# Performance work log

Hardware: AMD Instinct MI355X
Metric: run time of the kernel (lower is better)

The kernel has to match this reference:

```python
import jax, jax.numpy as jnp
import numpy as np

BOS = 1          # BOS_TOK_IDX
PAD = 0          # PAD_TOK_IDX (embedding padding row zeroed)
NL = 2           # n_layers (both decoder and encoder)
H_DEC = 1024     # decoder hidden = enc.emb_size
H_ENC = 512      # encoder hidden per direction (out_size = 1024)


def lstm_cell(x, h, c, Wih, Whh, bih, bhh):
    # PyTorch gate order: i, f, g, o
    gates = x @ Wih.T + h @ Whh.T + bih + bhh
    i, f, g, o = jnp.split(gates, 4, axis=-1)
    c = jax.nn.sigmoid(f) * c + jax.nn.sigmoid(i) * jnp.tanh(g)
    h = jax.nn.sigmoid(o) * jnp.tanh(c)
    return h, c


def setup_inputs() -> dict:
    key = jax.random.key(0)
    ks = jax.random.split(key, 20)
    B, T_ENC, V, E = 32, 128, 32000, 512
    sd = 1.0 / np.sqrt(H_DEC)
    se = 1.0 / np.sqrt(H_ENC)
    u = lambda k, shape, s: jax.random.uniform(k, shape, jnp.float32, -s, s)
    emb_W = jax.random.normal(ks[0], (V, E), jnp.float32)
    emb_W = emb_W.at[PAD].set(0.0)  # padding_idx
    return {
        "enc_outs": jax.random.normal(ks[1], (B, T_ENC, 2 * H_ENC), jnp.float32),
        "enc_h": 0.1 * jax.random.normal(ks[2], (NL, B, H_DEC), jnp.float32),
        "enc_c": 0.1 * jax.random.normal(ks[3], (NL, B, H_DEC), jnp.float32),
        "max_len": 256,
        "emb_W": emb_W,
        # decoder LSTM (unidirectional, 2 layers; layer0 in=E, layer1 in=H_DEC)
        "dec_Wih0": u(ks[4], (4 * H_DEC, E), sd),
        "dec_Whh0": u(ks[5], (4 * H_DEC, H_DEC), sd),
        "dec_bih0": u(ks[6], (4 * H_DEC,), sd),
        "dec_bhh0": u(ks[7], (4 * H_DEC,), sd),
        "dec_Wih1": u(ks[8], (4 * H_DEC, H_DEC), sd),
        "dec_Whh1": u(ks[9], (4 * H_DEC, H_DEC), sd),
        "dec_bih1": u(ks[10], (4 * H_DEC,), sd),
        "dec_bhh1": u(ks[11], (4 * H_DEC,), sd),
        # encoder biLSTM, stacked [layer, dir]; input dim 1024 for both layers
        "enc_Wih": u(ks[12], (NL, 2, 4 * H_ENC, 2 * H_ENC), se),
        "enc_Whh": u(ks[13], (NL, 2, 4 * H_ENC, H_ENC), se),
        "enc_bih": u(ks[14], (NL, 2, 4 * H_ENC), se),
        "enc_bhh": u(ks[15], (NL, 2, 4 * H_ENC), se),
    }


def _run_dir(x, Wih, Whh, bih, bhh, reverse):
    # x: [B, T, D] -> ys: [B, T, H], final (h, c)
    B = x.shape[0]
    H = Whh.shape[-1]
    z = jnp.zeros((B, H), dtype=x.dtype)

    def step(carry, xt):
        h, c = lstm_cell(xt, carry[0], carry[1], Wih, Whh, bih, bhh)
        return (h, c), h

    (hT, cT), ys = jax.lax.scan(step, (z, z), jnp.swapaxes(x, 0, 1), reverse=reverse)
    return jnp.swapaxes(ys, 0, 1), hT, cT


def reference(enc_outs, enc_h, enc_c, max_len, emb_W,
              dec_Wih0, dec_Whh0, dec_bih0, dec_bhh0,
              dec_Wih1, dec_Whh1, dec_bih1, dec_bhh1,
              enc_Wih, enc_Whh, enc_bih, enc_bhh):
    B = enc_outs.shape[0]
    # dec_inps is never updated in the loop: always the BOS embedding (eval dropout = id)
    x0 = jnp.broadcast_to(emb_W[BOS], (B, emb_W.shape[1]))

    def dec_step(carry, _):
        h0, c0, h1, c1 = carry
        h0, c0 = lstm_cell(x0, h0, c0, dec_Wih0, dec_Whh0, dec_bih0, dec_bhh0)
        h1, c1 = lstm_cell(h0, h1, c1, dec_Wih1, dec_Whh1, dec_bih1, dec_bhh1)
        return (h0, c0, h1, c1), h1

    init = (enc_h[0], enc_c[0], enc_h[1], enc_c[1])
    _, result = jax.lax.scan(dec_step, init, None, length=max_len)  # [T, B, H_DEC]
    out = jnp.swapaxes(result, 0, 1)  # [B, T, H_DEC]

    # bidirectional encoder over the decoded sequence (pre_embedded, full lengths)
    for l in range(NL):
        yf, hf, cf = _run_dir(out, enc_Wih[l, 0], enc_Whh[l, 0], enc_bih[l, 0], enc_bhh[l, 0], False)
        yb, hb, cb = _run_dir(out, enc_Wih[l, 1], enc_Whh[l, 1], enc_bih[l, 1], enc_bhh[l, 1], True)
        out = jnp.concatenate([yf, yb], axis=-1)

    # to_dec_state: concat last-layer fwd/bwd states, expand over n_layers
    lnhn = jnp.concatenate([hf, hb], axis=1)  # [B, out_size]
    lncn = jnp.concatenate([cf, cb], axis=1)
    dec_h = jnp.broadcast_to(lnhn, (NL,) + lnhn.shape)
    dec_c = jnp.broadcast_to(lncn, (NL,) + lncn.shape)
    return out, dec_h, dec_c
```

## Files before the change

### kernel.cpp

```cpp
#include <hip/hip_runtime.h>


typedef _Float16 f16;
typedef _Float16 hvec8 __attribute__((ext_vector_type(8)));
typedef float fvec4 __attribute__((ext_vector_type(4)));

#define WS_H0   4096
#define WS_H1   135168
#define WS_HE   266240
#define WS_DEC  397312
#define WS_Y0   17174528

__device__ __forceinline__ fvec4 mf(hvec8 a, hvec8 b, fvec4 c) {
    return __builtin_amdgcn_mfma_f32_16x16x32_f16(a, b, c, 0, 0, 0);
}

__device__ __forceinline__ hvec8 ldb8(const float* p) {
    hvec8 h;
#pragma unroll
    for (int j = 0; j < 8; ++j) h[j] = (f16)p[j];
    return h;
}

__device__ __forceinline__ hvec8 lda8(const f16* p) {
    hvec8 v;
    asm volatile("global_load_dwordx4 %0, %1, off sc1" : "=v"(v) : "v"(p));
    return v;
}
__device__ __forceinline__ void vm_wait() {
    asm volatile("s_waitcnt vmcnt(0)" ::: "memory");
    __builtin_amdgcn_sched_barrier(0);
}

__device__ __forceinline__ void st2(f16* p, float a, float b) {
    union { f16 h[2]; unsigned u; } x;
    x.h[0] = (f16)a; x.h[1] = (f16)b;
    __hip_atomic_store((unsigned*)p, x.u, __ATOMIC_RELAXED, __HIP_MEMORY_SCOPE_AGENT);
}

__device__ __forceinline__ float sigf(float x) { return 1.f / (1.f + __expf(-x)); }
__device__ __forceinline__ float thf(float x) {
    x = fminf(15.f, fmaxf(-15.f, x));
    float e = __expf(2.f * x);
    return (e - 1.f) / (e + 1.f);
}

#define RED(t, m, w, n)  red[(((t)*16 + (m))*132) + ((w)*16) + (n)]

__device__ __forceinline__ float sum8(const float* p) {
    return ((p[0] + p[16]) + (p[32] + p[48])) + ((p[64] + p[80]) + (p[96] + p[112]));
}

__global__ void __launch_bounds__(512, 1)
seq2seq_kernel(const float* __restrict__ enc_h, const float* __restrict__ enc_c,
               const float* __restrict__ emb_W,
               const float* __restrict__ dWih0, const float* __restrict__ dWhh0,
               const float* __restrict__ dbih0, const float* __restrict__ dbhh0,
               const float* __restrict__ dWih1, const float* __restrict__ dWhh1,
               const float* __restrict__ dbih1, const float* __restrict__ dbhh1,
               const float* __restrict__ eWih, const float* __restrict__ eWhh,
               const float* __restrict__ ebih, const float* __restrict__ ebhh,
               float* __restrict__ out, char* __restrict__ ws)
{
    const int tid  = threadIdx.x;
    const int wave = tid >> 6, lane = tid & 63;
    const int wg   = blockIdx.x;
    const int bg   = wg >> 7;
    const int g    = wg & 127;
    const int n16  = lane & 15;
    const int kq   = (lane >> 4) * 8;

    unsigned* flags  = (unsigned*)ws;
    unsigned* myflag = flags + (size_t)wg * 4;

    f16* H0  = (f16*)(ws + WS_H0);
    f16* H1  = (f16*)(ws + WS_H1);
    f16* HE  = (f16*)(ws + WS_HE);
    f16* DEC = (f16*)(ws + WS_DEC);
    f16* Y0  = (f16*)(ws + WS_Y0);

    __shared__ float red[64 * 132];
    __shared__ float cdec[2][8][16];
    __shared__ float cenc[16][16];
    __shared__ float pre0_l[32];
    __shared__ float bias1_l[32];
    __shared__ float biasE_l[64];

    unsigned cnt = 0;
    auto bar = [&](int base, int width) {
        const unsigned tgt = ++cnt;
        __syncthreads();
        if (wave == 0) {
            if (lane == 0)
                __hip_atomic_store(myflag, tgt, __ATOMIC_RELAXED, __HIP_MEMORY_SCOPE_AGENT);
            const unsigned* p0 = flags + (size_t)(base + (lane & (width - 1))) * 4;
            for (;;) {
                unsigned a = __hip_atomic_load(p0, __ATOMIC_RELAXED, __HIP_MEMORY_SCOPE_AGENT);
                if (width > 64) {
                    unsigned b = __hip_atomic_load(p0 + 64 * 4, __ATOMIC_RELAXED, __HIP_MEMORY_SCOPE_AGENT);
                    a = a < b ? a : b;
                    if (width > 128) {
                        unsigned c2 = __hip_atomic_load(p0 + 128 * 4, __ATOMIC_RELAXED, __HIP_MEMORY_SCOPE_AGENT);
                        unsigned d2 = __hip_atomic_load(p0 + 192 * 4, __ATOMIC_RELAXED, __HIP_MEMORY_SCOPE_AGENT);
                        a = a < c2 ? a : c2;
                        a = a < d2 ? a : d2;
                    }
                }
                if (__all((int)(a >= tgt))) break;
            }
        }
        __syncthreads();
    };

    const int u0 = g * 8;
    hvec8 bL0[2][4], bL1[2][8];
    {
        const int gate = n16 >> 2, uu = n16 & 3;
#pragma unroll
        for (int t = 0; t < 2; ++t) {
            const int r = gate * 1024 + u0 + t * 4 + uu;
#pragma unroll
            for (int s = 0; s < 4; ++s)
                bL0[t][s] = ldb8(dWhh0 + (size_t)r * 1024 + wave * 128 + s * 32 + kq);
#pragma unroll
            for (int s = 0; s < 8; ++s) {
                const int k1 = wave * 256 + s * 32;
                bL1[t][s] = (k1 < 1024)
                    ? ldb8(dWih1 + (size_t)r * 1024 + k1 + kq)
                    : ldb8(dWhh1 + (size_t)r * 1024 + (k1 - 1024) + kq);
            }
        }
    }
    if (tid < 128) {
        const int which = tid >> 6, q = tid & 63, j = q >> 4, m = q & 15;
        const int b = bg * 16 + m, u = u0 + 2 * j;
        const float* src_c = enc_c + (size_t)(which * 32 + b) * 1024 + u;
        const float* src_h = enc_h + (size_t)(which * 32 + b) * 1024 + u;
        cdec[which][2 * j][m]     = src_c[0];
        cdec[which][2 * j + 1][m] = src_c[1];
        f16* dst = which ? H1 : H0;
        st2(dst + (size_t)(32 + b) * 1024 + u, src_h[0], src_h[1]);
    }
    if (tid < 32) {
        const int t = tid >> 4, nn = tid & 15;
        const int r = (nn >> 2) * 1024 + u0 + t * 4 + (nn & 3);
        const float* x0 = emb_W + 512;
        float s = dbih0[r] + dbhh0[r];
        const float* wr = dWih0 + (size_t)r * 512;
        for (int k = 0; k < 512; ++k) s += wr[k] * x0[k];
        pre0_l[tid]  = s;
        bias1_l[tid] = dbih1[r] + dbhh1[r];
    }
    bar(bg * 128, 128);

    for (int tau = 0; tau <= 256; ++tau) {
        const int prd = (tau + 1) & 1;
        const int pwr = tau & 1;
        fvec4 acc[4];
#pragma unroll
        for (int i = 0; i < 4; ++i) acc[i] = 0;
        const int m = n16;
        hvec8 a0f[4], a1f[8];
        if (tau < 256) {
            const f16* a0 = H0 + (size_t)(prd * 32 + bg * 16 + m) * 1024 + wave * 128 + kq;
#pragma unroll
            for (int s = 0; s < 4; ++s) a0f[s] = lda8(a0 + s * 32);
        }
        if (tau >= 1) {
            const f16* a1 = (wave < 4)
                ? H0 + (size_t)(prd * 32 + bg * 16 + m) * 1024 + wave * 256 + kq
                : H1 + (size_t)(pwr * 32 + bg * 16 + m) * 1024 + (wave - 4) * 256 + kq;
#pragma unroll
            for (int s = 0; s < 8; ++s) a1f[s] = lda8(a1 + s * 32);
        }
        vm_wait();
        if (tau < 256) {
#pragma unroll
            for (int s = 0; s < 4; ++s) {
                acc[0] = mf(a0f[s], bL0[0][s], acc[0]);
                acc[1] = mf(a0f[s], bL0[1][s], acc[1]);
            }
        }
        if (tau >= 1) {
#pragma unroll
            for (int s = 0; s < 8; ++s) {
                acc[2] = mf(a1f[s], bL1[0][s], acc[2]);
                acc[3] = mf(a1f[s], bL1[1][s], acc[3]);
            }
        }
        {
            const int mg = lane >> 4;
#pragma unroll
            for (int t = 0; t < 4; ++t)
#pragma unroll
                for (int r = 0; r < 4; ++r)
                    RED(t, mg * 4 + r, wave, n16) = acc[t][r];
        }
        __syncthreads();
        if (tid < 64 && tau < 256) {
            const int j = tid >> 4, m2 = tid & 15, t = j >> 1;
            float hh[2];
#pragma unroll
            for (int e = 0; e < 2; ++e) {
                const int uu = 2 * j + e, ul = uu & 3;
                const float* p = &RED(t, m2, 0, ul);
                const float gi = sum8(p)      + pre0_l[t * 16 + ul];
                const float gf = sum8(p + 4)  + pre0_l[t * 16 + 4 + ul];
                const float gg = sum8(p + 8)  + pre0_l[t * 16 + 8 + ul];
                const float go = sum8(p + 12) + pre0_l[t * 16 + 12 + ul];
                float c = cdec[0][uu][m2];
                c = sigf(gf) * c + sigf(gi) * thf(gg);
                hh[e] = sigf(go) * thf(c);
                cdec[0][uu][m2] = c;
            }
            st2(H0 + (size_t)(pwr * 32 + bg * 16 + m2) * 1024 + u0 + 2 * j, hh[0], hh[1]);
        }
        if (tid >= 64 && tid < 128 && tau >= 1) {
            const int q = tid - 64;
            const int j = q >> 4, m2 = q & 15, t = j >> 1;
            float hh[2];
#pragma unroll
            for (int e = 0; e < 2; ++e) {
                const int uu = 2 * j + e, ul = uu & 3;
                const float* p = &RED(2 + t, m2, 0, ul);
                const float gi = sum8(p)      + bias1_l[t * 16 + ul];
                const float gf = sum8(p + 4)  + bias1_l[t * 16 + 4 + ul];
                const float gg = sum8(p + 8)  + bias1_l[t * 16 + 8 + ul];
                const float go = sum8(p + 12) + bias1_l[t * 16 + 12 + ul];
                float c = cdec[1][uu][m2];
                c = sigf(gf) * c + sigf(gi) * thf(gg);
                hh[e] = sigf(go) * thf(c);
                cdec[1][uu][m2] = c;
            }
            const int b = bg * 16 + m2, u = u0 + 2 * j;
            st2(H1 + (size_t)(prd * 32 + b) * 1024 + u, hh[0], hh[1]);
            st2(DEC + ((size_t)(tau - 1) * 32 + b) * 1024 + u, hh[0], hh[1]);
        }
        bar(bg * 128, 128);
    }

    bar(0, 256);
    if (wg >= 128) return;

    const int bg2 = wg >> 6;
    const int dir = (wg >> 5) & 1;
    const int ge  = wg & 31;
    const int ue0 = ge * 16;
    const int dbase = bg2 * 64 + dir * 32;
    for (int l = 0; l < 2; ++l) {
        hvec8 bE[4][6];
        {
            const int gate = n16 >> 2, uu = n16 & 3;
            const float* Wih = eWih + (size_t)(l * 2 + dir) * 2048 * 1024;
            const float* Whh = eWhh + (size_t)(l * 2 + dir) * 2048 * 512;
#pragma unroll
            for (int t = 0; t < 4; ++t) {
                const int r = gate * 512 + ue0 + t * 4 + uu;
#pragma unroll
                for (int s = 0; s < 6; ++s) {
                    const int kb = wave * 192 + s * 32;
                    bE[t][s] = (kb < 1024)
                        ? ldb8(Wih + (size_t)r * 1024 + kb + kq)
                        : ldb8(Whh + (size_t)r * 512 + (kb - 1024) + kq);
                }
            }
        }
        if (tid < 64) {
            const int t = tid >> 4, nn = tid & 15;
            const int r = (nn >> 2) * 512 + ue0 + t * 4 + (nn & 3);
            biasE_l[tid] = ebih[(size_t)(l * 2 + dir) * 2048 + r]
                         + ebhh[(size_t)(l * 2 + dir) * 2048 + r];
        }
        if (tid < 128) {
            const int j = tid >> 4, m = tid & 15;
            cenc[2 * j][m] = 0.f;
            cenc[2 * j + 1][m] = 0.f;
            st2(HE + (size_t)((dir * 2 + 1) * 32 + bg2 * 16 + m) * 512 + ue0 + 2 * j, 0.f, 0.f);
        }
        bar(dbase, 32);
        const f16* yprev = (l == 0) ? DEC : Y0;
        hvec8 ypf[6];
        {
            const int t0 = dir ? 255 : 0;
            const int b = bg2 * 16 + n16;
#pragma unroll
            for (int s = 0; s < 6; ++s) {
                const int kb = wave * 192 + s * 32;
                if (kb < 1024)
                    ypf[s] = lda8(yprev + ((size_t)t0 * 32 + b) * 1024 + kb + kq);
            }
        }
        for (int tau = 0; tau < 256; ++tau) {
            const int t = dir ? (255 - tau) : tau;
            const int prd = (tau + 1) & 1, pwr = tau & 1;
            const int b = bg2 * 16 + n16;
            hvec8 hef[6];
#pragma unroll
            for (int s = 0; s < 6; ++s) {
                const int kb = wave * 192 + s * 32;
                if (kb >= 1024)
                    hef[s] = lda8(HE + (size_t)((dir * 2 + prd) * 32 + b) * 512 + (kb - 1024) + kq);
            }
            vm_wait();
            fvec4 acc2[4];
#pragma unroll
            for (int i = 0; i < 4; ++i) acc2[i] = 0;
#pragma unroll
            for (int s = 0; s < 6; ++s) {
                const int kb = wave * 192 + s * 32;
                const hvec8 a = (kb < 1024) ? ypf[s] : hef[s];
                acc2[0] = mf(a, bE[0][s], acc2[0]);
                acc2[1] = mf(a, bE[1][s], acc2[1]);
                acc2[2] = mf(a, bE[2][s], acc2[2]);
                acc2[3] = mf(a, bE[3][s], acc2[3]);
            }
            if (tau < 255) {
                const int tn = dir ? (t - 1) : (t + 1);
#pragma unroll
                for (int s = 0; s < 6; ++s) {
                    const int kb = wave * 192 + s * 32;
                    if (kb < 1024)
                        ypf[s] = lda8(yprev + ((size_t)tn * 32 + b) * 1024 + kb + kq);
                }
            }
            const int mg = lane >> 4;
#pragma unroll
            for (int tt = 0; tt < 4; ++tt)
#pragma unroll
                for (int r = 0; r < 4; ++r)
                    RED(tt, mg * 4 + r, wave, n16) = acc2[tt][r];
            __syncthreads();
            if (tid < 128) {
                const int j = tid >> 4, m2 = tid & 15;
                float hh[2], cc[2];
#pragma unroll
                for (int e = 0; e < 2; ++e) {
                    const int uu = 2 * j + e, tt = uu >> 2, ul = uu & 3;
                    const float* p = &RED(tt, m2, 0, ul);
                    const float gi = sum8(p)      + biasE_l[tt * 16 + ul];
                    const float gf = sum8(p + 4)  + biasE_l[tt * 16 + 4 + ul];
                    const float gg = sum8(p + 8)  + biasE_l[tt * 16 + 8 + ul];
                    const float go = sum8(p + 12) + biasE_l[tt * 16 + 12 + ul];
                    float c = cenc[uu][m2];
                    c = sigf(gf) * c + sigf(gi) * thf(gg);
                    hh[e] = sigf(go) * thf(c);
                    cc[e] = c;
                    cenc[uu][m2] = c;
                }
                const int b2 = bg2 * 16 + m2, u = ue0 + 2 * j;
                st2(HE + (size_t)((dir * 2 + pwr) * 32 + b2) * 512 + u, hh[0], hh[1]);
                if (l == 0) {
                    st2(Y0 + ((size_t)t * 32 + b2) * 1024 + dir * 512 + u, hh[0], hh[1]);
                } else {
                    float* o = out + ((size_t)b2 * 256 + t) * 1024 + dir * 512 + u;
                    o[0] = hh[0]; o[1] = hh[1];
                    if (tau == 255) {
                        const int col = dir * 512 + u;
                        float* oh = out + 8388608 + (size_t)b2 * 1024 + col;
                        float* oc = out + 8454144 + (size_t)b2 * 1024 + col;
                        oh[0] = hh[0]; oh[1] = hh[1];
                        oh[32768] = hh[0]; oh[32769] = hh[1];
                        oc[0] = cc[0]; oc[1] = cc[1];
                        oc[32768] = cc[0]; oc[32769] = cc[1];
                    }
                }
            }
            bar(dbase, 32);
        }
        if (l == 0) bar(bg2 * 64, 64);
    }
}

extern "C" void kernel_launch(void* const* d_in, const int* in_sizes, int n_in,
                              void* d_out, int out_size, void* d_ws, size_t ws_size,
                              hipStream_t stream) {
    (void)in_sizes; (void)n_in; (void)out_size; (void)ws_size;
    const float* enc_h = (const float*)d_in[1];
    const float* enc_c = (const float*)d_in[2];
    const float* emb_W = (const float*)d_in[4];
    const float* dWih0 = (const float*)d_in[5];
    const float* dWhh0 = (const float*)d_in[6];
    const float* dbih0 = (const float*)d_in[7];
    const float* dbhh0 = (const float*)d_in[8];
    const float* dWih1 = (const float*)d_in[9];
    const float* dWhh1 = (const float*)d_in[10];
    const float* dbih1 = (const float*)d_in[11];
    const float* dbhh1 = (const float*)d_in[12];
    const float* eWih  = (const float*)d_in[13];
    const float* eWhh  = (const float*)d_in[14];
    const float* ebih  = (const float*)d_in[15];
    const float* ebhh  = (const float*)d_in[16];
    float* outp = (float*)d_out;
    char* ws = (char*)d_ws;

    hipMemsetAsync(d_ws, 0, 4096, stream);

    void* args[] = {&enc_h, &enc_c, &emb_W, &dWih0, &dWhh0, &dbih0, &dbhh0,
                    &dWih1, &dWhh1, &dbih1, &dbhh1, &eWih, &eWhh, &ebih, &ebhh,
                    &outp, &ws};
    hipLaunchCooperativeKernel((const void*)seq2seq_kernel, dim3(256), dim3(512),
                               args, 0, stream);
}
```

Measured before the change: 3.791 ms.

## Pad barrier flags to separate lines and overlap output stores with grid barrier

```diff
diff --git a/kernel.cpp b/kernel.cpp
--- a/kernel.cpp
+++ b/kernel.cpp
@@ -70,8 +70,8 @@
     const int n16  = lane & 15;
     const int kq   = (lane >> 4) * 8;
 
-    unsigned* flags  = (unsigned*)ws;
-    unsigned* myflag = flags + (size_t)wg * 4;
+    unsigned* flags  = (unsigned*)(out + 8388608);
+    unsigned* myflag = flags + (size_t)wg * 64;
 
     f16* H0  = (f16*)(ws + WS_H0);
     f16* H1  = (f16*)(ws + WS_H1);
@@ -87,29 +87,25 @@
     __shared__ float biasE_l[64];
 
     unsigned cnt = 0;
-    auto bar = [&](int base, int width) {
-        const unsigned tgt = ++cnt;
-        __syncthreads();
-        if (wave == 0) {
-            if (lane == 0)
-                __hip_atomic_store(myflag, tgt, __ATOMIC_RELAXED, __HIP_MEMORY_SCOPE_AGENT);
-            const unsigned* p0 = flags + (size_t)(base + (lane & (width - 1))) * 4;
-            for (;;) {
-                unsigned a = __hip_atomic_load(p0, __ATOMIC_RELAXED, __HIP_MEMORY_SCOPE_AGENT);
-                if (width > 64) {
-                    unsigned b = __hip_atomic_load(p0 + 64 * 4, __ATOMIC_RELAXED, __HIP_MEMORY_SCOPE_AGENT);
-                    a = a < b ? a : b;
-                    if (width > 128) {
-                        unsigned c2 = __hip_atomic_load(p0 + 128 * 4, __ATOMIC_RELAXED, __HIP_MEMORY_SCOPE_AGENT);
-                        unsigned d2 = __hip_atomic_load(p0 + 192 * 4, __ATOMIC_RELAXED, __HIP_MEMORY_SCOPE_AGENT);
-                        a = a < c2 ? a : c2;
-                        a = a < d2 ? a : d2;
-                    }
+    auto barpoll = [&](int base, int width, unsigned tgt) {
+        if (lane == 0)
+            __hip_atomic_store(myflag, tgt, __ATOMIC_RELAXED, __HIP_MEMORY_SCOPE_AGENT);
+        const unsigned* p0 = flags + (size_t)(base + (lane & (width - 1))) * 64;
+        for (;;) {
+            unsigned a = __hip_atomic_load(p0, __ATOMIC_RELAXED, __HIP_MEMORY_SCOPE_AGENT);
+            if (width > 64) {
+                unsigned b = __hip_atomic_load(p0 + 64 * 64, __ATOMIC_RELAXED, __HIP_MEMORY_SCOPE_AGENT);
+                a = a < b ? a : b;
+                if (width > 128) {
+                    unsigned c2 = __hip_atomic_load(p0 + 128 * 64, __ATOMIC_RELAXED, __HIP_MEMORY_SCOPE_AGENT);
+                    unsigned d2 = __hip_atomic_load(p0 + 192 * 64, __ATOMIC_RELAXED, __HIP_MEMORY_SCOPE_AGENT);
+                    a = a < c2 ? a : c2;
+                    a = a < d2 ? a : d2;
                 }
-                if (__all((int)(a >= tgt))) break;
-            }
-        }
-        __syncthreads();
+            }
+            if (__all((int)(a >= tgt))) break;
+            __builtin_amdgcn_s_sleep(1);
+        }
     };
 
     const int u0 = g * 8;
@@ -151,7 +147,9 @@
         pre0_l[tid]  = s;
         bias1_l[tid] = dbih1[r] + dbhh1[r];
     }
-    bar(bg * 128, 128);
+    __syncthreads();
+    if (wave == 0) barpoll(bg * 128, 128, ++cnt);
+    __syncthreads();
 
     for (int tau = 0; tau <= 256; ++tau) {
         const int prd = (tau + 1) & 1;
@@ -197,8 +195,11 @@
                     RED(t, mg * 4 + r, wave, n16) = acc[t][r];
         }
         __syncthreads();
-        if (tid < 64 && tau < 256) {
-            const int j = tid >> 4, m2 = tid & 15, t = j >> 1;
+        float s0 = 0.f, s1 = 0.f;
+        int   sm2 = 0, sj = 0;
+        if (wave == 1 && tau < 256) {
+            const int q = tid - 64;
+            const int j = q >> 4, m2 = q & 15, t = j >> 1;
             float hh[2];
 #pragma unroll
             for (int e = 0; e < 2; ++e) {
@@ -215,8 +216,8 @@
             }
             st2(H0 + (size_t)(pwr * 32 + bg * 16 + m2) * 1024 + u0 + 2 * j, hh[0], hh[1]);
         }
-        if (tid >= 64 && tid < 128 && tau >= 1) {
-            const int q = tid - 64;
+        if (wave == 2 && tau >= 1) {
+            const int q = tid - 128;
             const int j = q >> 4, m2 = q & 15, t = j >> 1;
             float hh[2];
 #pragma unroll
@@ -234,12 +235,20 @@
             }
             const int b = bg * 16 + m2, u = u0 + 2 * j;
             st2(H1 + (size_t)(prd * 32 + b) * 1024 + u, hh[0], hh[1]);
-            st2(DEC + ((size_t)(tau - 1) * 32 + b) * 1024 + u, hh[0], hh[1]);
-        }
-        bar(bg * 128, 128);
-    }
-
-    bar(0, 256);
+            s0 = hh[0]; s1 = hh[1]; sm2 = m2; sj = j;
+        }
+        __syncthreads();
+        if (wave == 0) {
+            barpoll(bg * 128, 128, ++cnt);
+        } else if (wave == 2 && tau >= 1) {
+            st2(DEC + ((size_t)(tau - 1) * 32 + bg * 16 + sm2) * 1024 + u0 + 2 * sj, s0, s1);
+        }
+        __syncthreads();
+    }
+
+    __syncthreads();
+    if (wave == 0) barpoll(0, 256, ++cnt);
+    __syncthreads();
     if (wg >= 128) return;
 
     const int bg2 = wg >> 6;
@@ -247,6 +256,8 @@
     const int ge  = wg & 31;
     const int ue0 = ge * 16;
     const int dbase = bg2 * 64 + dir * 32;
+    float fdh0 = 0.f, fdh1 = 0.f, fdc0 = 0.f, fdc1 = 0.f;
+    int   fdm2 = 0, fdj = 0;
     for (int l = 0; l < 2; ++l) {
         hvec8 bE[4][6];
         {
@@ -277,7 +288,9 @@
             cenc[2 * j + 1][m] = 0.f;
             st2(HE + (size_t)((dir * 2 + 1) * 32 + bg2 * 16 + m) * 512 + ue0 + 2 * j, 0.f, 0.f);
         }
-        bar(dbase, 32);
+        __syncthreads();
+        if (wave == 0) barpoll(dbase, 32, ++cnt);
+        __syncthreads();
         const f16* yprev = (l == 0) ? DEC : Y0;
         hvec8 ypf[6];
         {
@@ -330,8 +343,11 @@
                 for (int r = 0; r < 4; ++r)
                     RED(tt, mg * 4 + r, wave, n16) = acc2[tt][r];
             __syncthreads();
-            if (tid < 128) {
-                const int j = tid >> 4, m2 = tid & 15;
+            float dh0 = 0.f, dh1 = 0.f, dc0 = 0.f, dc1 = 0.f;
+            int   dm2 = 0, dj = 0;
+            if (tid >= 64 && tid < 192) {
+                const int q = tid - 64;
+                const int j = q >> 4, m2 = q & 15;
                 float hh[2], cc[2];
 #pragma unroll
                 for (int e = 0; e < 2; ++e) {
@@ -347,27 +363,48 @@
                     cc[e] = c;
                     cenc[uu][m2] = c;
                 }
-                const int b2 = bg2 * 16 + m2, u = ue0 + 2 * j;
-                st2(HE + (size_t)((dir * 2 + pwr) * 32 + b2) * 512 + u, hh[0], hh[1]);
+                st2(HE + (size_t)((dir * 2 + pwr) * 32 + bg2 * 16 + m2) * 512 + ue0 + 2 * j,
+                    hh[0], hh[1]);
+                dh0 = hh[0]; dh1 = hh[1]; dc0 = cc[0]; dc1 = cc[1];
+                dm2 = m2; dj = j;
+            }
+            __syncthreads();
+            if (wave == 0) {
+                if (!(l == 1 && tau == 255)) barpoll(dbase, 32, ++cnt);
+            } else if (tid >= 64 && tid < 192) {
+                const int b2 = bg2 * 16 + dm2, u = ue0 + 2 * dj;
                 if (l == 0) {
-                    st2(Y0 + ((size_t)t * 32 + b2) * 1024 + dir * 512 + u, hh[0], hh[1]);
+                    st2(Y0 + ((size_t)t * 32 + b2) * 1024 + dir * 512 + u, dh0, dh1);
                 } else {
                     float* o = out + ((size_t)b2 * 256 + t) * 1024 + dir * 512 + u;
-                    o[0] = hh[0]; o[1] = hh[1];
+                    o[0] = dh0; o[1] = dh1;
                     if (tau == 255) {
-                        const int col = dir * 512 + u;
-                        float* oh = out + 8388608 + (size_t)b2 * 1024 + col;
-                        float* oc = out + 8454144 + (size_t)b2 * 1024 + col;
-                        oh[0] = hh[0]; oh[1] = hh[1];
-                        oh[32768] = hh[0]; oh[32769] = hh[1];
-                        oc[0] = cc[0]; oc[1] = cc[1];
-                        oc[32768] = cc[0]; oc[32769] = cc[1];
+                        fdh0 = dh0; fdh1 = dh1;
+                        fdc0 = dc0; fdc1 = dc1;
+                        fdm2 = dm2; fdj = dj;
                     }
                 }
             }
-            bar(dbase, 32);
-        }
-        if (l == 0) bar(bg2 * 64, 64);
+            __syncthreads();
+        }
+        if (l == 0) {
+            __syncthreads();
+            if (wave == 0) barpoll(bg2 * 64, 64, ++cnt);
+            __syncthreads();
+        }
+    }
+    __syncthreads();
+    if (wave == 0) barpoll(0, 128, ++cnt);
+    __syncthreads();
+    if (tid >= 64 && tid < 192) {
+        const int b2 = bg2 * 16 + fdm2;
+        const int col = dir * 512 + ue0 + 2 * fdj;
+        float* oh = out + 8388608 + (size_t)b2 * 1024 + col;
+        float* oc = out + 8454144 + (size_t)b2 * 1024 + col;
+        oh[0] = fdh0; oh[1] = fdh1;
+        oh[32768] = fdh0; oh[32769] = fdh1;
+        oc[0] = fdc0; oc[1] = fdc1;
+        oc[32768] = fdc0; oc[32769] = fdc1;
     }
 }
 
@@ -393,7 +430,7 @@
     float* outp = (float*)d_out;
     char* ws = (char*)d_ws;
 
-    hipMemsetAsync(d_ws, 0, 4096, stream);
+    hipMemsetAsync((char*)d_out + 33554432, 0, 65536, stream);
 
     void* args[] = {&enc_h, &enc_c, &emb_W, &dWih0, &dWhh0, &dbih0, &dbhh0,
                     &dWih1, &dWhh1, &dbih1, &dbhh1, &eWih, &eWhh, &ebih, &ebhh,
```

Result: faster. 3.552 ms (-6.3%).
